# Kernel optimization log

Measured on AMD Instinct MI355X. Metric: run time of the kernel, lower is better.

Reference implementation:

```python
import jax, jax.numpy as jnp
import numpy as np

RADIUS = 5          # box-filter radius -> 11x11 kernel
TEMP = 0.5          # multinomial temperature
NSAMP = 5           # sampling_num
EPS = 1e-6
BN_EPS = 1e-5


def _conv(x, w, stride=1, padding=0, groups=1):
    return jax.lax.conv_general_dilated(
        x, w, window_strides=(stride, stride),
        padding=[(padding, padding), (padding, padding)],
        feature_group_count=groups,
        dimension_numbers=("NCHW", "OIHW", "NCHW"))


def custom_conv(x, w, key, stride=1, padding=0):
    """conv2d with cosine-activation regularization (bias=False path)."""
    B = x.shape[0]
    Cout = w.shape[0]
    # all-ones 'norm' conv on x*x
    x_norm = jnp.sqrt(_conv(x * x, jnp.ones_like(w), stride, padding))
    y = _conv(x, w, stride, padding)
    w_norm = jnp.sqrt(jnp.sum(w * w, axis=(1, 2, 3)))  # per-out-channel Frobenius norm
    cosine = y / (w_norm[None, :, None, None] + EPS) / (x_norm + EPS)
    # 11x11 depthwise box filter
    k = 2 * RADIUS + 1
    dw = jnp.ones((Cout, 1, k, k), x.dtype)
    cosine_mean = _conv(cosine, dw, 1, RADIUS, groups=Cout) / (k * k)
    H, W = cosine.shape[2], cosine.shape[3]
    # multinomial(NSAMP, exp(cosine/TEMP)) counts, no_grad in original
    logits = jax.lax.stop_gradient(cosine).reshape(B, Cout, H * W) / TEMP
    idx = jax.random.categorical(key, logits, axis=-1, shape=(NSAMP, B, Cout))
    bi = jnp.broadcast_to(jnp.arange(B)[None, :, None], (NSAMP, B, Cout))
    ci = jnp.broadcast_to(jnp.arange(Cout)[None, None, :], (NSAMP, B, Cout))
    mask = jnp.zeros((B, Cout, H * W), x.dtype).at[bi, ci, idx].add(1.0)
    cm = cosine_mean.reshape(B, Cout, H * W)
    act = ((mask * cm).sum(-1) / mask.sum(-1)).mean()
    return y, act


def batchnorm(x, g, b):
    # training-mode batch statistics (biased variance), like nn.BatchNorm2d
    m = x.mean(axis=(0, 2, 3), keepdims=True)
    v = x.var(axis=(0, 2, 3), keepdims=True)
    return (x - m) / jnp.sqrt(v + BN_EPS) * g[None, :, None, None] + b[None, :, None, None]


def setup_inputs() -> dict:
    key = jax.random.key(0)
    ks = jax.random.split(key, 10)
    x = jax.random.normal(ks[0], (16, 256, 56, 56), jnp.float32)
    w1 = jax.random.normal(ks[1], (64, 256, 1, 1), jnp.float32) * 0.05
    w2 = jax.random.normal(ks[2], (64, 64, 3, 3), jnp.float32) * 0.05
    w3 = jax.random.normal(ks[3], (256, 64, 1, 1), jnp.float32) * 0.05
    g1 = 1.0 + 0.05 * jax.random.normal(ks[4], (64,), jnp.float32)
    b1 = 0.05 * jax.random.normal(ks[5], (64,), jnp.float32)
    g2 = 1.0 + 0.05 * jax.random.normal(ks[6], (64,), jnp.float32)
    b2 = 0.05 * jax.random.normal(ks[7], (64,), jnp.float32)
    g3 = 1.0 + 0.05 * jax.random.normal(ks[8], (256,), jnp.float32)
    b3 = 0.05 * jax.random.normal(ks[9], (256,), jnp.float32)
    return {"x": x, "w1": w1, "w2": w2, "w3": w3,
            "g1": g1, "b1": b1, "g2": g2, "b2": b2, "g3": g3, "b3": b3}


def reference(x, w1, w2, w3, g1, b1, g2, b2, g3, b3):
    k0, k1, k2 = jax.random.split(jax.random.key(42), 3)
    acc = jnp.asarray(0.0, x.dtype)
    out, a = custom_conv(x, w1, k0)           # conv1x1
    acc = acc + a
    out = jax.nn.relu(batchnorm(out, g1, b1))
    out, a = custom_conv(out, w2, k1, padding=1)  # conv3x3, stride 1
    acc = acc + a
    out = jax.nn.relu(batchnorm(out, g2, b2))
    out, a = custom_conv(out, w3, k2)         # conv1x1 expand
    acc = acc + a
    out = batchnorm(out, g3, b3)
    out = jax.nn.relu(out + x)                # identity shortcut (downsample=None)
    return out, acc
```

## Files before the change

### kernel.cpp

```cpp
#include <hip/hip_runtime.h>
#include <stdint.h>
#include <math.h>

#define HW 3136
#define NPIX 50176

__device__ __forceinline__ int min_i(int a, int b) { return a < b ? a : b; }

typedef __attribute__((ext_vector_type(8))) short bf16x8;
typedef __attribute__((ext_vector_type(4))) float f32x4;
#define MFMA16(a, b, c) __builtin_amdgcn_mfma_f32_16x16x32_bf16(a, b, c, 0, 0, 0)

__device__ __forceinline__ unsigned short f2bf(float f) {
  unsigned u = __float_as_uint(f);
  u = (u + 0x7fffu + ((u >> 16) & 1u)) >> 16;
  return (unsigned short)u;
}
__device__ __forceinline__ unsigned pk2(float a, float b) {
  return (unsigned)f2bf(a) | ((unsigned)f2bf(b) << 16);
}
__device__ __forceinline__ float bf2f(unsigned short h) {
  return __uint_as_float(((unsigned)h) << 16);
}

#define ROTL32(v, r) __builtin_rotateleft32((uint32_t)(v), (r))

__host__ __device__ inline void threefry2x32(uint32_t k0, uint32_t k1,
                                             uint32_t x0, uint32_t x1,
                                             uint32_t& o0, uint32_t& o1) {
  uint32_t k2 = k0 ^ k1 ^ 0x1BD11BDAu;
  x0 += k0; x1 += k1;
  x0 += x1; x1 = ROTL32(x1, 13); x1 ^= x0;
  x0 += x1; x1 = ROTL32(x1, 15); x1 ^= x0;
  x0 += x1; x1 = ROTL32(x1, 26); x1 ^= x0;
  x0 += x1; x1 = ROTL32(x1, 6);  x1 ^= x0;
  x0 += k1; x1 += k2 + 1u;
  x0 += x1; x1 = ROTL32(x1, 17); x1 ^= x0;
  x0 += x1; x1 = ROTL32(x1, 29); x1 ^= x0;
  x0 += x1; x1 = ROTL32(x1, 16); x1 ^= x0;
  x0 += x1; x1 = ROTL32(x1, 24); x1 ^= x0;
  x0 += k2; x1 += k0 + 2u;
  x0 += x1; x1 = ROTL32(x1, 13); x1 ^= x0;
  x0 += x1; x1 = ROTL32(x1, 15); x1 ^= x0;
  x0 += x1; x1 = ROTL32(x1, 26); x1 ^= x0;
  x0 += x1; x1 = ROTL32(x1, 6);  x1 ^= x0;
  x0 += k0; x1 += k1 + 3u;
  x0 += x1; x1 = ROTL32(x1, 17); x1 ^= x0;
  x0 += x1; x1 = ROTL32(x1, 29); x1 ^= x0;
  x0 += x1; x1 = ROTL32(x1, 16); x1 ^= x0;
  x0 += x1; x1 = ROTL32(x1, 24); x1 ^= x0;
  x0 += k1; x1 += k2 + 4u;
  x0 += x1; x1 = ROTL32(x1, 13); x1 ^= x0;
  x0 += x1; x1 = ROTL32(x1, 15); x1 ^= x0;
  x0 += x1; x1 = ROTL32(x1, 26); x1 ^= x0;
  x0 += x1; x1 = ROTL32(x1, 6);  x1 ^= x0;
  x0 += k2; x1 += k0 + 5u;
  o0 = x0; o1 = x1;
}

#define TF5_R(r)                                            \
  _Pragma("unroll") for (int i = 0; i < 5; ++i) {           \
    x0[i] += x1[i]; x1[i] = ROTL32(x1[i], r) ^ x0[i];       \
  }
#define TF5_INJ(a, b)                                       \
  _Pragma("unroll") for (int i = 0; i < 5; ++i) {           \
    x0[i] += (a); x1[i] += (b);                             \
  }
__device__ __forceinline__ void threefry5(uint32_t k0, uint32_t k1,
    const uint32_t xa[5], const uint32_t xb[5], uint32_t oa[5], uint32_t ob[5]) {
  uint32_t k2 = k0 ^ k1 ^ 0x1BD11BDAu;
  uint32_t x0[5], x1[5];
  #pragma unroll
  for (int i = 0; i < 5; ++i) { x0[i] = xa[i] + k0; x1[i] = xb[i] + k1; }
  TF5_R(13) TF5_R(15) TF5_R(26) TF5_R(6)  TF5_INJ(k1, k2 + 1u)
  TF5_R(17) TF5_R(29) TF5_R(16) TF5_R(24) TF5_INJ(k2, k0 + 2u)
  TF5_R(13) TF5_R(15) TF5_R(26) TF5_R(6)  TF5_INJ(k0, k1 + 3u)
  TF5_R(17) TF5_R(29) TF5_R(16) TF5_R(24) TF5_INJ(k1, k2 + 4u)
  TF5_R(13) TF5_R(15) TF5_R(26) TF5_R(6)  TF5_INJ(k2, k0 + 5u)
  #pragma unroll
  for (int i = 0; i < 5; ++i) { oa[i] = x0[i]; ob[i] = x1[i]; }
}

#define NLN2F -0.6931471805599453f
#define NEG2LOG2E -2.8853900817779268f
__device__ __forceinline__ float exp_draw(uint32_t bits) {
  float u = __uint_as_float((bits >> 9) | 0x3f800000u) - 1.0f;
  u = fmaxf(u, 1.17549435e-38f);
  return NLN2F * __log2f(u);
}

template <int NT>
__device__ void sample5_body(const unsigned short* __restrict__ CS,
    float* __restrict__ acc, uint32_t key0, uint32_t key1, int BC, float scale,
    int u, unsigned* kmin, float* wsum) {
  const int v = u + (BC >> 1);
  const uint32_t sC = (uint32_t)BC * (uint32_t)HW;
  const uint32_t halfn = sC * 2u + (sC >> 1);
  const unsigned short* rowU = CS + (size_t)u * HW;
  const unsigned short* rowV = CS + (size_t)v * HW;
  const int tid = threadIdx.x;
  const int lane = tid & 63;

  if (tid < 10) { kmin[tid] = 0xFFFFFFFFu; wsum[tid] = 0.f; }

  unsigned bk[10];
  #pragma unroll
  for (int k = 0; k < 10; ++k) bk[k] = 0xFFFFFFFFu;

  const uint32_t baseU0 = (uint32_t)u * (uint32_t)HW;
  const uint32_t baseV0 = (uint32_t)v * (uint32_t)HW;
  for (int p = tid; p < HW; p += NT) {
    float wu = __builtin_amdgcn_exp2f(bf2f(rowU[p]) * NEG2LOG2E);
    float wv = __builtin_amdgcn_exp2f(bf2f(rowV[p]) * NEG2LOG2E);
    uint32_t eU = baseU0 + (uint32_t)p;
    uint32_t eV = baseV0 + (uint32_t)p;
    uint32_t xa[5] = {eU, eU + sC, eU + 2 * sC, eV, eV + sC};
    uint32_t xb[5] = {eU + halfn, eU + sC + halfn, eU + 2 * sC + halfn,
                      eV + halfn, eV + sC + halfn};
    uint32_t oa[5], ob[5];
    threefry5(key0, key1, xa, xb, oa, ob);
    uint32_t wds[10] = {oa[0], oa[1], oa[2], ob[3], ob[4],
                        oa[3], oa[4], ob[0], ob[1], ob[2]};
    #pragma unroll
    for (int k = 0; k < 10; ++k) {
      float s = exp_draw(wds[k]) * (k < 5 ? wu : wv);
      unsigned key = (__float_as_uint(s) & 0xFFFFF000u) | (unsigned)p;
      bk[k] = bk[k] < key ? bk[k] : key;
    }
  }

  __syncthreads();
  #pragma unroll
  for (int k = 0; k < 10; ++k) {
    unsigned kv = bk[k];
    #pragma unroll
    for (int o = 32; o; o >>= 1) {
      unsigned ov = __shfl_xor(kv, o);
      kv = kv < ov ? kv : ov;
    }
    if (lane == 0) atomicMin(&kmin[k], kv);
  }
  __syncthreads();

  for (int idx = tid; idx < 1210; idx += NT) {
    int win = idx / 121, j = idx - win * 121;
    int bidx = (int)(kmin[win] & 0xFFFu);
    int py = bidx / 56, px = bidx % 56;
    int yy = py + j / 11 - 5, xx = px + j % 11 - 5;
    if (yy >= 0 && yy < 56 && xx >= 0 && xx < 56) {
      const unsigned short* row = (win < 5) ? rowU : rowV;
      atomicAdd(&wsum[win], bf2f(row[yy * 56 + xx]));
    }
  }
  __syncthreads();
  if (tid == 0) {
    float t = 0.f;
    #pragma unroll
    for (int k = 0; k < 10; ++k) t += wsum[k];
    atomicAdd(acc, t * scale);
  }
}

template <int NT>
__global__ __launch_bounds__(NT) void sample5_k(const unsigned short* __restrict__ CS,
    float* __restrict__ acc, uint32_t key0, uint32_t key1, int BC, float scale) {
  __shared__ unsigned kmin[10];
  __shared__ float wsum[10];
  sample5_body<NT>(CS, acc, key0, key1, BC, scale, blockIdx.x, kmin, wsum);
}

__global__ void wprep_k(const float* __restrict__ w1, const float* __restrict__ w2,
                        const float* __restrict__ w3, float* __restrict__ invwn,
                        unsigned short* __restrict__ W1b, unsigned short* __restrict__ W2tb,
                        unsigned short* __restrict__ W3b) {
  int i = blockIdx.x * 256 + threadIdx.x;
  if (i < 16384) {
    W1b[i] = f2bf(w1[i]);
  } else if (i < 53248) {
    int o = i - 16384;
    int co = o / 576, r = o % 576, tap = r >> 6, ci = r & 63;
    W2tb[o] = f2bf(w2[co * 576 + ci * 9 + tap]);
  } else if (i < 69632) {
    int o = i - 53248;
    W3b[o] = f2bf(w3[o]);
  } else {
    int t = i - 69632;
    if (t < 64) {
      float s = 0.f;
      for (int k = 0; k < 256; k++) { float v = w1[t * 256 + k]; s = fmaf(v, v, s); }
      invwn[t] = 1.0f / (sqrtf(s) + 1e-6f);
    } else if (t < 128) {
      int c = t - 64; float s = 0.f;
      for (int k = 0; k < 576; k++) { float v = w2[c * 576 + k]; s = fmaf(v, v, s); }
      invwn[t] = 1.0f / (sqrtf(s) + 1e-6f);
    } else if (t < 384) {
      int c = t - 128; float s = 0.f;
      for (int k = 0; k < 64; k++) { float v = w3[c * 64 + k]; s = fmaf(v, v, s); }
      invwn[t] = 1.0f / (sqrtf(s) + 1e-6f);
    }
  }
}

__global__ __launch_bounds__(256) void bn_fin(const float* __restrict__ Sp,
    const float* __restrict__ Qp, const float* __restrict__ g,
    const float* __restrict__ b, float* __restrict__ sc, float* __restrict__ sh,
    int nblk) {
  const int c = blockIdx.x, tid = threadIdx.x;
  const float* rs = Sp + (size_t)c * nblk;
  const float* rq = Qp + (size_t)c * nblk;
  float s = 0.f, q = 0.f;
  for (int i = tid; i < nblk; i += 256) { s += rs[i]; q += rq[i]; }
  #pragma unroll
  for (int o = 32; o; o >>= 1) { s += __shfl_xor(s, o); q += __shfl_xor(q, o); }
  __shared__ float S[4], Q[4];
  int lane = tid & 63, wave = tid >> 6;
  if (lane == 0) { S[wave] = s; Q[wave] = q; }
  __syncthreads();
  if (tid == 0) {
    float st = S[0] + S[1] + S[2] + S[3];
    float qt = Q[0] + Q[1] + Q[2] + Q[3];
    float mean = st * (1.0f / (float)NPIX);
    float var = qt * (1.0f / (float)NPIX) - mean * mean;
    float sv = g[c] / sqrtf(var + 1e-5f);
    sc[c] = sv; sh[c] = b[c] - mean * sv;
  }
}

__global__ __launch_bounds__(256) void conv1_mfma(
    const float* __restrict__ X, const unsigned short* __restrict__ Wb,
    const float* __restrict__ invwn, unsigned short* __restrict__ Y1,
    unsigned short* __restrict__ CS, float* __restrict__ Sp, float* __restrict__ Qp) {
#define ST1 264
#define NB1 784
  __shared__ __align__(16) unsigned short bq[64 * ST1];
  __shared__ float sqp[4][64];
  __shared__ float ixn[64];
  const int p0 = blockIdx.x * 64, b = blockIdx.y;
  const int bid = b * 49 + blockIdx.x;
  const int tid = threadIdx.x;
  const int lane = tid & 63, wave = tid >> 6;
  const int m = lane & 15, quad = lane >> 4;
  const int co0 = wave * 16;
  const float* Xb = X + (size_t)b * 256 * HW + p0;

  bf16x8 afr[8];
  const unsigned short* wrow = Wb + (co0 + m) * 256 + quad * 8;
  #pragma unroll
  for (int k = 0; k < 8; ++k) afr[k] = *(const bf16x8*)(wrow + k * 32);

  {
    const int px = tid & 63, rg = tid >> 6;
    float sq = 0.f;
    #pragma unroll
    for (int it = 0; it < 16; ++it) {
      int ci = rg * 64 + it * 4;
      float v0 = Xb[(size_t)(ci + 0) * HW + px];
      float v1 = Xb[(size_t)(ci + 1) * HW + px];
      float v2 = Xb[(size_t)(ci + 2) * HW + px];
      float v3 = Xb[(size_t)(ci + 3) * HW + px];
      sq += v0 * v0 + v1 * v1 + v2 * v2 + v3 * v3;
      *(uint2*)&bq[px * ST1 + ci] = make_uint2(pk2(v0, v1), pk2(v2, v3));
    }
    sqp[rg][px] = sq;
  }
  __syncthreads();
  if (tid < 64)
    ixn[tid] = 1.0f / (sqrtf(sqp[0][tid] + sqp[1][tid] + sqp[2][tid] + sqp[3][tid]) + 1e-6f);
  __syncthreads();

  f32x4 acc[4];
  #pragma unroll
  for (int nt = 0; nt < 4; ++nt) acc[nt] = (f32x4)0.f;
  #pragma unroll
  for (int nt = 0; nt < 4; ++nt) {
    const unsigned short* brow = &bq[(nt * 16 + m) * ST1 + quad * 8];
    #pragma unroll
    for (int k = 0; k < 8; ++k) {
      bf16x8 bfrag = *(const bf16x8*)(brow + k * 32);
      acc[nt] = MFMA16(afr[k], bfrag, acc[nt]);
    }
  }

  float s[4] = {0, 0, 0, 0}, q[4] = {0, 0, 0, 0};
  #pragma unroll
  for (int nt = 0; nt < 4; ++nt) {
    int px = nt * 16 + m;
    size_t bp = (size_t)b * HW + p0 + px;
    float ix = ixn[px];
    *(uint2*)&Y1[bp * 64 + co0 + quad * 4] =
        make_uint2(pk2(acc[nt][0], acc[nt][1]), pk2(acc[nt][2], acc[nt][3]));
    #pragma unroll
    for (int r = 0; r < 4; ++r) {
      int co = co0 + quad * 4 + r;
      float v = acc[nt][r];
      CS[((size_t)b * 64 + co) * HW + p0 + px] = f2bf(v * invwn[co] * ix);
      s[r] += v; q[r] = fmaf(v, v, q[r]);
    }
  }
  #pragma unroll
  for (int r = 0; r < 4; ++r) {
    float ss = s[r], qq = q[r];
    #pragma unroll
    for (int o = 8; o; o >>= 1) { ss += __shfl_xor(ss, o); qq += __shfl_xor(qq, o); }
    if (m == 0) {
      int co = co0 + quad * 4 + r;
      Sp[(size_t)co * NB1 + bid] = ss; Qp[(size_t)co * NB1 + bid] = qq;
    }
  }
#undef NB1
#undef ST1
}

__global__ __launch_bounds__(256) void chansum_px(const unsigned short* __restrict__ Y1,
    const float* __restrict__ sc, const float* __restrict__ sh,
    float* __restrict__ part) {
  int g = blockIdx.x * 256 + threadIdx.x;
  const unsigned short* row = Y1 + (size_t)g * 64;
  float s = 0.f;
  #pragma unroll
  for (int j = 0; j < 8; ++j) {
    uint4 d = *(const uint4*)(row + j * 8);
    unsigned dd[4] = {d.x, d.y, d.z, d.w};
    #pragma unroll
    for (int e = 0; e < 4; ++e) {
      int c = j * 8 + e * 2;
      float v0 = fmaxf(0.f, fmaf(bf2f((unsigned short)(dd[e] & 0xffff)), sc[c], sh[c]));
      float v1 = fmaxf(0.f, fmaf(bf2f((unsigned short)(dd[e] >> 16)), sc[c + 1], sh[c + 1]));
      s = fmaf(v0, v0, s); s = fmaf(v1, v1, s);
    }
  }
  part[g] = s;
}

__global__ __launch_bounds__(256) void box3inv(const float* __restrict__ part,
                                               float* __restrict__ out) {
  int g = blockIdx.x * 256 + threadIdx.x;
  int b = g / HW, p = g - b * HW;
  int y = p / 56, x = p % 56;
  float tot = 0.f;
  for (int dy = -1; dy <= 1; dy++) {
    int yy = y + dy; if (yy < 0 || yy >= 56) continue;
    for (int dx = -1; dx <= 1; dx++) {
      int xx = x + dx; if (xx < 0 || xx >= 56) continue;
      tot += part[b * HW + yy * 56 + xx];
    }
  }
  out[g] = 1.0f / (sqrtf(tot) + 1e-6f);
}

__global__ __launch_bounds__(256) void conv2_mfma(
    const unsigned short* __restrict__ Y1, const unsigned short* __restrict__ W2tb,
    const float* __restrict__ invwn, const float* __restrict__ ixn2,
    const float* __restrict__ sc1, const float* __restrict__ sh1,
    unsigned short* __restrict__ Y2, unsigned short* __restrict__ CS,
    float* __restrict__ Sp, float* __restrict__ Qp) {
#define STW 72
#define NB2 896
  __shared__ __align__(16) unsigned short ts[3 * 66 * STW];
  __shared__ float scl[64], shl[64];
  const int h = blockIdx.x, b = blockIdx.y;
  const int bid = b * 56 + h;
  const int tid = threadIdx.x;
  const int lane = tid & 63, wave = tid >> 6;
  const int m = lane & 15, quad = lane >> 4;
  const int co0 = wave * 16;
  if (tid < 64) { scl[tid] = sc1[tid]; shl[tid] = sh1[tid]; }

  bf16x8 afr[18];
  #pragma unroll
  for (int ks = 0; ks < 18; ++ks)
    afr[ks] = *(const bf16x8*)(W2tb + (co0 + m) * 576 + ks * 32 + quad * 8);
  __syncthreads();

  for (int l = tid; l < 6336; l += 256) {
    int cp = l & 31, cc = (l >> 5) % 66, dy = l / 2112;
    int yy = h - 1 + dy, xx = cc - 1;
    unsigned pkv = 0u;
    if (yy >= 0 && yy < 56 && xx >= 0 && xx < 56) {
      unsigned d = *(const unsigned*)&Y1[((size_t)b * HW + yy * 56 + xx) * 64 + cp * 2];
      float v0 = bf2f((unsigned short)(d & 0xffff));
      float v1 = bf2f((unsigned short)(d >> 16));
      v0 = fmaxf(0.f, fmaf(v0, scl[cp * 2], shl[cp * 2]));
      v1 = fmaxf(0.f, fmaf(v1, scl[cp * 2 + 1], shl[cp * 2 + 1]));
      pkv = pk2(v0, v1);
    }
    *(unsigned*)&ts[(dy * 66 + cc) * STW + cp * 2] = pkv;
  }
  __syncthreads();

  f32x4 acc[4];
  #pragma unroll
  for (int nt = 0; nt < 4; ++nt) acc[nt] = (f32x4)0.f;
  #pragma unroll
  for (int nt = 0; nt < 4; ++nt) {
    #pragma unroll
    for (int ks = 0; ks < 18; ++ks) {
      int tap = ks >> 1, half = ks & 1;
      int dy = tap / 3, dx = tap % 3;
      bf16x8 bfrag = *(const bf16x8*)&ts[(dy * 66 + nt * 16 + m + dx) * STW + half * 32 + quad * 8];
      acc[nt] = MFMA16(afr[ks], bfrag, acc[nt]);
    }
  }

  float s[4] = {0, 0, 0, 0}, q[4] = {0, 0, 0, 0};
  #pragma unroll
  for (int nt = 0; nt < 4; ++nt) {
    int px = nt * 16 + m;
    bool valid = px < 56;
    int pix = h * 56 + px;
    if (valid) {
      float ix = ixn2[b * HW + pix];
      size_t bp = (size_t)b * HW + pix;
      *(uint2*)&Y2[bp * 64 + co0 + quad * 4] =
          make_uint2(pk2(acc[nt][0], acc[nt][1]), pk2(acc[nt][2], acc[nt][3]));
      #pragma unroll
      for (int r = 0; r < 4; ++r) {
        int co = co0 + quad * 4 + r;
        CS[((size_t)b * 64 + co) * HW + pix] = f2bf(acc[nt][r] * invwn[co] * ix);
      }
    }
    #pragma unroll
    for (int r = 0; r < 4; ++r) {
      float v = valid ? acc[nt][r] : 0.f;
      s[r] += v; q[r] = fmaf(v, v, q[r]);
    }
  }
  #pragma unroll
  for (int r = 0; r < 4; ++r) {
    float ss = s[r], qq = q[r];
    #pragma unroll
    for (int o = 8; o; o >>= 1) { ss += __shfl_xor(ss, o); qq += __shfl_xor(qq, o); }
    if (m == 0) {
      int co = co0 + quad * 4 + r;
      Sp[(size_t)co * NB2 + bid] = ss; Qp[(size_t)co * NB2 + bid] = qq;
    }
  }
#undef NB2
#undef STW
}

__global__ __launch_bounds__(256) void conv3_mfma(
    const unsigned short* __restrict__ Y2, const unsigned short* __restrict__ W3b,
    const float* __restrict__ invwn,
    const float* __restrict__ sc2, const float* __restrict__ sh2,
    unsigned short* __restrict__ Y3, unsigned short* __restrict__ CS,
    float* __restrict__ Sp, float* __restrict__ Qp) {
#define ST3 72
#define NB3 784
  __shared__ __align__(16) unsigned short bq[64 * ST3];
  __shared__ float scl[64], shl[64], sqp[4][64], ixn[64];
  const int p0 = blockIdx.x * 64, b = blockIdx.y;
  const int bid = b * 49 + blockIdx.x;
  const int tid = threadIdx.x;
  const int lane = tid & 63, wave = tid >> 6;
  const int m = lane & 15, quad = lane >> 4;
  const int co0 = wave * 64;
  if (tid < 64) { scl[tid] = sc2[tid]; shl[tid] = sh2[tid]; }

  bf16x8 afr[4][2];
  #pragma unroll
  for (int mt = 0; mt < 4; ++mt)
    #pragma unroll
    for (int k = 0; k < 2; ++k)
      afr[mt][k] = *(const bf16x8*)(W3b + (co0 + mt * 16 + m) * 64 + k * 32 + quad * 8);
  __syncthreads();

  {
    const int cp = tid & 31, pxg = tid >> 5;
    #pragma unroll
    for (int it = 0; it < 8; ++it) {
      int px = pxg * 8 + it;
      unsigned d = *(const unsigned*)&Y2[((size_t)b * HW + p0 + px) * 64 + cp * 2];
      float v0 = bf2f((unsigned short)(d & 0xffff));
      float v1 = bf2f((unsigned short)(d >> 16));
      v0 = fmaxf(0.f, fmaf(v0, scl[cp * 2], shl[cp * 2]));
      v1 = fmaxf(0.f, fmaf(v1, scl[cp * 2 + 1], shl[cp * 2 + 1]));
      *(unsigned*)&bq[px * ST3 + cp * 2] = pk2(v0, v1);
    }
  }
  __syncthreads();
  {
    const int px = tid & 63, hh = tid >> 6;
    const unsigned short* row = &bq[px * ST3 + hh * 16];
    float sq = 0.f;
    #pragma unroll
    for (int e = 0; e < 16; ++e) { float v = bf2f(row[e]); sq = fmaf(v, v, sq); }
    sqp[hh][px] = sq;
  }
  __syncthreads();
  if (tid < 64)
    ixn[tid] = 1.0f / (sqrtf(sqp[0][tid] + sqp[1][tid] + sqp[2][tid] + sqp[3][tid]) + 1e-6f);
  __syncthreads();

  f32x4 acc[4][4];
  #pragma unroll
  for (int mt = 0; mt < 4; ++mt)
    #pragma unroll
    for (int nt = 0; nt < 4; ++nt) acc[mt][nt] = (f32x4)0.f;
  #pragma unroll
  for (int nt = 0; nt < 4; ++nt) {
    const unsigned short* brow = &bq[(nt * 16 + m) * ST3 + quad * 8];
    bf16x8 b0 = *(const bf16x8*)(brow);
    bf16x8 b1 = *(const bf16x8*)(brow + 32);
    #pragma unroll
    for (int mt = 0; mt < 4; ++mt) {
      acc[mt][nt] = MFMA16(afr[mt][0], b0, acc[mt][nt]);
      acc[mt][nt] = MFMA16(afr[mt][1], b1, acc[mt][nt]);
    }
  }

  #pragma unroll
  for (int mt = 0; mt < 4; ++mt) {
    float s[4] = {0, 0, 0, 0}, q[4] = {0, 0, 0, 0};
    #pragma unroll
    for (int nt = 0; nt < 4; ++nt) {
      int px = nt * 16 + m;
      float ix = ixn[px];
      #pragma unroll
      for (int r = 0; r < 4; ++r) {
        int co = co0 + mt * 16 + quad * 4 + r;
        float v = acc[mt][nt][r];
        size_t off = ((size_t)b * 256 + co) * HW + p0 + px;
        Y3[off] = f2bf(v);
        CS[off] = f2bf(v * invwn[co] * ix);
        s[r] += v; q[r] = fmaf(v, v, q[r]);
      }
    }
    #pragma unroll
    for (int r = 0; r < 4; ++r) {
      float ss = s[r], qq = q[r];
      #pragma unroll
      for (int o = 8; o; o >>= 1) { ss += __shfl_xor(ss, o); qq += __shfl_xor(qq, o); }
      if (m == 0) {
        int co = co0 + mt * 16 + quad * 4 + r;
        Sp[(size_t)co * NB3 + bid] = ss; Qp[(size_t)co * NB3 + bid] = qq;
      }
    }
  }
#undef NB3
#undef ST3
}

__global__ __launch_bounds__(256, 8) void final_samp_fused(
    const unsigned short* __restrict__ Y3, const float* __restrict__ X,
    const float* __restrict__ sc, const float* __restrict__ sh,
    float* __restrict__ out, const unsigned short* __restrict__ CS3,
    float* __restrict__ accp, uint32_t key0, uint32_t key1, float scale,
    int NS, int R) {
  __shared__ unsigned kmin[10];
  __shared__ float wsum[10];
  const int g = blockIdx.x;
  if ((g % R) == 0 && (g / R) < NS) {
    sample5_body<256>(CS3, accp, key0, key1, 4096, scale, g / R, kmin, wsum);
    return;
  }
  const int fb = g - min_i((g + R - 1) / R, NS);
  size_t i4 = (size_t)fb * 256 + threadIdx.x;
  size_t i = i4 * 4;
  int c = (int)((i / HW) % 256);
  float a = sc[c], d = sh[c];
  uint2 yd = *(const uint2*)&Y3[i];
  float4 xv = *(const float4*)&X[i];
  float4 r;
  r.x = fmaxf(0.f, fmaf(bf2f((unsigned short)(yd.x & 0xffff)), a, d) + xv.x);
  r.y = fmaxf(0.f, fmaf(bf2f((unsigned short)(yd.x >> 16)),    a, d) + xv.y);
  r.z = fmaxf(0.f, fmaf(bf2f((unsigned short)(yd.y & 0xffff)), a, d) + xv.z);
  r.w = fmaxf(0.f, fmaf(bf2f((unsigned short)(yd.y >> 16)),    a, d) + xv.w);
  *(float4*)&out[i] = r;
}

__global__ void acc_write_k(const float* __restrict__ accp, float* __restrict__ out) {
  out[12845056] = accp[0];
}

extern "C" void kernel_launch(void* const* d_in, const int* in_sizes, int n_in,
                              void* d_out, int out_size, void* d_ws, size_t ws_size,
                              hipStream_t stream) {
  (void)in_sizes; (void)n_in; (void)out_size; (void)ws_size;
  const float* x  = (const float*)d_in[0];
  const float* w1 = (const float*)d_in[1];
  const float* w2 = (const float*)d_in[2];
  const float* w3 = (const float*)d_in[3];
  const float* g1 = (const float*)d_in[4];
  const float* b1 = (const float*)d_in[5];
  const float* g2 = (const float*)d_in[6];
  const float* b2 = (const float*)d_in[7];
  const float* g3 = (const float*)d_in[8];
  const float* b3 = (const float*)d_in[9];
  float* out = (float*)d_out;
  float* ws = (float*)d_ws;

  size_t o = 0;
  unsigned short* y3b  = (unsigned short*)(ws + o); o += 6422528;
  unsigned short* cos3 = (unsigned short*)(ws + o); o += 6422528;
  unsigned short* CSb  = (unsigned short*)(ws + o); o += 1605632;
  unsigned short* y1b  = (unsigned short*)(ws + o); o += 1605632;
  unsigned short* y2b  = (unsigned short*)(ws + o); o += 1605632;
  unsigned short* W1b  = (unsigned short*)(ws + o); o += 8192;
  unsigned short* W2tb = (unsigned short*)(ws + o); o += 18432;
  unsigned short* W3b  = (unsigned short*)(ws + o); o += 8192;
  float* part = ws + o; o += NPIX;
  float* ixn2 = ws + o; o += NPIX;
  float* invwn = ws + o; o += 384;
  float* Sp1 = ws + o; o += 64 * 784;   float* Qp1 = ws + o; o += 64 * 784;
  float* Sp2 = ws + o; o += 64 * 896;   float* Qp2 = ws + o; o += 64 * 896;
  float* Sp3 = ws + o; o += 256 * 784;  float* Qp3 = ws + o; o += 256 * 784;
  float* acc = ws + o; o += 1;
  float* sc1 = ws + o; o += 64;  float* sh1 = ws + o; o += 64;
  float* sc2 = ws + o; o += 64;  float* sh2 = ws + o; o += 64;
  float* sc3 = ws + o; o += 256; float* sh3 = ws + o; o += 256;

  hipMemsetAsync(acc, 0, sizeof(float), stream);

  uint32_t A0, B0, A1, B1, A2, B2;
  threefry2x32(0u, 42u, 0u, 3u, A0, B0);
  threefry2x32(0u, 42u, 1u, 4u, A1, B1);
  threefry2x32(0u, 42u, 2u, 5u, A2, B2);

  const float scale64  = 1.0f / (121.0f * 5.0f * 1024.0f);
  const float scale256 = 1.0f / (121.0f * 5.0f * 4096.0f);

  wprep_k<<<274, 256, 0, stream>>>(w1, w2, w3, invwn, W1b, W2tb, W3b);

  conv1_mfma<<<dim3(49, 16), 256, 0, stream>>>(x, W1b, invwn, y1b, CSb, Sp1, Qp1);
  bn_fin<<<64, 256, 0, stream>>>(Sp1, Qp1, g1, b1, sc1, sh1, 784);
  sample5_k<512><<<512, 512, 0, stream>>>(CSb, acc, A0, A1, 1024, scale64);

  chansum_px<<<196, 256, 0, stream>>>(y1b, sc1, sh1, part);
  box3inv<<<196, 256, 0, stream>>>(part, ixn2);
  conv2_mfma<<<dim3(56, 16), 256, 0, stream>>>(
      y1b, W2tb, invwn + 64, ixn2, sc1, sh1, y2b, CSb, Sp2, Qp2);
  bn_fin<<<64, 256, 0, stream>>>(Sp2, Qp2, g2, b2, sc2, sh2, 896);
  sample5_k<512><<<512, 512, 0, stream>>>(CSb, acc, A2, B0, 1024, scale64);

  conv3_mfma<<<dim3(49, 16), 256, 0, stream>>>(
      y2b, W3b, invwn + 128, sc2, sh2, y3b, cos3, Sp3, Qp3);
  bn_fin<<<256, 256, 0, stream>>>(Sp3, Qp3, g3, b3, sc3, sh3, 784);

  final_samp_fused<<<14592, 256, 0, stream>>>(
      y3b, x, sc3, sh3, out, cos3, acc, B1, B2, scale256, 2048, 2);
  acc_write_k<<<1, 1, 0, stream>>>(acc, out);
}
```

Before: 451.6 us.

## Defer all three sampling passes into one fused final kernel

When the workspace is large enough, the conv2 cosine map goes to a separate buffer, so the two stage-1/2 sampling launches can be deferred. All three multinomial sampling passes then run in one final kernel alongside the BN+residual+ReLU elementwise work. This removes two serialized launches and lets sampling overlap the bandwidth-bound epilogue. In exchange it uses more workspace, and each sampling block loops over two (batch, channel) pairs with 256 threads instead of 512.

Result: faster. 402.4 us (-10.9%).

```diff
diff --git a/kernel.cpp b/kernel.cpp
--- a/kernel.cpp
+++ b/kernel.cpp
@@ -4,8 +4,6 @@
 
 #define HW 3136
 #define NPIX 50176
-
-__device__ __forceinline__ int min_i(int a, int b) { return a < b ? a : b; }
 
 typedef __attribute__((ext_vector_type(8))) short bf16x8;
 typedef __attribute__((ext_vector_type(4))) float f32x4;
@@ -169,6 +167,47 @@
   sample5_body<NT>(CS, acc, key0, key1, BC, scale, blockIdx.x, kmin, wsum);
 }
 
+__global__ __launch_bounds__(256, 8) void mega_k(
+    const unsigned short* __restrict__ CS1, const unsigned short* __restrict__ CS2,
+    const unsigned short* __restrict__ CS3,
+    const unsigned short* __restrict__ Y3, const float* __restrict__ X,
+    const float* __restrict__ sc, const float* __restrict__ sh,
+    float* __restrict__ out, float* __restrict__ accp,
+    uint32_t A0, uint32_t A1, uint32_t A2, uint32_t B0, uint32_t B1, uint32_t B2,
+    float s64, float s256, int pairStart, int pairEnd, int nSampBlk, int NF) {
+  __shared__ unsigned kmin[10];
+  __shared__ float wsum[10];
+  const int g = blockIdx.x;
+  if (g < nSampBlk) {
+    for (int pi = pairStart + g; pi < pairEnd; pi += nSampBlk) {
+      if (pi < 512)
+        sample5_body<256>(CS1, accp, A0, A1, 1024, s64, pi, kmin, wsum);
+      else if (pi < 1024)
+        sample5_body<256>(CS2, accp, A2, B0, 1024, s64, pi - 512, kmin, wsum);
+      else
+        sample5_body<256>(CS3, accp, B1, B2, 4096, s256, pi - 1024, kmin, wsum);
+    }
+    return;
+  }
+  const int fb = g - nSampBlk;
+  if (fb >= NF) return;
+  size_t i = ((size_t)fb * 256 + threadIdx.x) * 4;
+  int c = (int)((i / HW) % 256);
+  float a = sc[c], d = sh[c];
+  uint2 yd = *(const uint2*)&Y3[i];
+  float4 xv = *(const float4*)&X[i];
+  float4 r;
+  r.x = fmaxf(0.f, fmaf(bf2f((unsigned short)(yd.x & 0xffff)), a, d) + xv.x);
+  r.y = fmaxf(0.f, fmaf(bf2f((unsigned short)(yd.x >> 16)),    a, d) + xv.y);
+  r.z = fmaxf(0.f, fmaf(bf2f((unsigned short)(yd.y & 0xffff)), a, d) + xv.z);
+  r.w = fmaxf(0.f, fmaf(bf2f((unsigned short)(yd.y >> 16)),    a, d) + xv.w);
+  *(float4*)&out[i] = r;
+}
+
+__global__ void acc_write_k(const float* __restrict__ accp, float* __restrict__ out) {
+  out[12845056] = accp[0];
+}
+
 __global__ void wprep_k(const float* __restrict__ w1, const float* __restrict__ w2,
                         const float* __restrict__ w3, float* __restrict__ invwn,
                         unsigned short* __restrict__ W1b, unsigned short* __restrict__ W2tb,
@@ -541,42 +580,10 @@
 #undef ST3
 }
 
-__global__ __launch_bounds__(256, 8) void final_samp_fused(
-    const unsigned short* __restrict__ Y3, const float* __restrict__ X,
-    const float* __restrict__ sc, const float* __restrict__ sh,
-    float* __restrict__ out, const unsigned short* __restrict__ CS3,
-    float* __restrict__ accp, uint32_t key0, uint32_t key1, float scale,
-    int NS, int R) {
-  __shared__ unsigned kmin[10];
-  __shared__ float wsum[10];
-  const int g = blockIdx.x;
-  if ((g % R) == 0 && (g / R) < NS) {
-    sample5_body<256>(CS3, accp, key0, key1, 4096, scale, g / R, kmin, wsum);
-    return;
-  }
-  const int fb = g - min_i((g + R - 1) / R, NS);
-  size_t i4 = (size_t)fb * 256 + threadIdx.x;
-  size_t i = i4 * 4;
-  int c = (int)((i / HW) % 256);
-  float a = sc[c], d = sh[c];
-  uint2 yd = *(const uint2*)&Y3[i];
-  float4 xv = *(const float4*)&X[i];
-  float4 r;
-  r.x = fmaxf(0.f, fmaf(bf2f((unsigned short)(yd.x & 0xffff)), a, d) + xv.x);
-  r.y = fmaxf(0.f, fmaf(bf2f((unsigned short)(yd.x >> 16)),    a, d) + xv.y);
-  r.z = fmaxf(0.f, fmaf(bf2f((unsigned short)(yd.y & 0xffff)), a, d) + xv.z);
-  r.w = fmaxf(0.f, fmaf(bf2f((unsigned short)(yd.y >> 16)),    a, d) + xv.w);
-  *(float4*)&out[i] = r;
-}
-
-__global__ void acc_write_k(const float* __restrict__ accp, float* __restrict__ out) {
-  out[12845056] = accp[0];
-}
-
 extern "C" void kernel_launch(void* const* d_in, const int* in_sizes, int n_in,
                               void* d_out, int out_size, void* d_ws, size_t ws_size,
                               hipStream_t stream) {
-  (void)in_sizes; (void)n_in; (void)out_size; (void)ws_size;
+  (void)in_sizes; (void)n_in; (void)out_size;
   const float* x  = (const float*)d_in[0];
   const float* w1 = (const float*)d_in[1];
   const float* w2 = (const float*)d_in[2];
@@ -610,6 +617,9 @@
   float* sc2 = ws + o; o += 64;  float* sh2 = ws + o; o += 64;
   float* sc3 = ws + o; o += 256; float* sh3 = ws + o; o += 256;
 
+  const bool big = ws_size >= (o + 1605632) * sizeof(float);
+  unsigned short* CS2b = big ? (unsigned short*)(ws + o) : CSb;
+
   hipMemsetAsync(acc, 0, sizeof(float), stream);
 
   uint32_t A0, B0, A1, B1, A2, B2;
@@ -624,20 +634,27 @@
 
   conv1_mfma<<<dim3(49, 16), 256, 0, stream>>>(x, W1b, invwn, y1b, CSb, Sp1, Qp1);
   bn_fin<<<64, 256, 0, stream>>>(Sp1, Qp1, g1, b1, sc1, sh1, 784);
-  sample5_k<512><<<512, 512, 0, stream>>>(CSb, acc, A0, A1, 1024, scale64);
-
+  if (!big)
+    sample5_k<512><<<512, 512, 0, stream>>>(CSb, acc, A0, A1, 1024, scale64);
   chansum_px<<<196, 256, 0, stream>>>(y1b, sc1, sh1, part);
   box3inv<<<196, 256, 0, stream>>>(part, ixn2);
   conv2_mfma<<<dim3(56, 16), 256, 0, stream>>>(
-      y1b, W2tb, invwn + 64, ixn2, sc1, sh1, y2b, CSb, Sp2, Qp2);
+      y1b, W2tb, invwn + 64, ixn2, sc1, sh1, y2b, CS2b, Sp2, Qp2);
   bn_fin<<<64, 256, 0, stream>>>(Sp2, Qp2, g2, b2, sc2, sh2, 896);
-  sample5_k<512><<<512, 512, 0, stream>>>(CSb, acc, A2, B0, 1024, scale64);
-
+  if (!big)
+    sample5_k<512><<<512, 512, 0, stream>>>(CS2b, acc, A2, B0, 1024, scale64);
   conv3_mfma<<<dim3(49, 16), 256, 0, stream>>>(
       y2b, W3b, invwn + 128, sc2, sh2, y3b, cos3, Sp3, Qp3);
   bn_fin<<<256, 256, 0, stream>>>(Sp3, Qp3, g3, b3, sc3, sh3, 784);
 
-  final_samp_fused<<<14592, 256, 0, stream>>>(
-      y3b, x, sc3, sh3, out, cos3, acc, B1, B2, scale256, 2048, 2);
+  if (big) {
+    mega_k<<<1536 + 12544, 256, 0, stream>>>(
+        CSb, CS2b, cos3, y3b, x, sc3, sh3, out, acc,
+        A0, A1, A2, B0, B1, B2, scale64, scale256, 0, 3072, 1536, 12544);
+  } else {
+    mega_k<<<1024 + 12544, 256, 0, stream>>>(
+        CSb, CS2b, cos3, y3b, x, sc3, sh3, out, acc,
+        A0, A1, A2, B0, B1, B2, scale64, scale256, 1024, 3072, 1024, 12544);
+  }
   acc_write_k<<<1, 1, 0, stream>>>(acc, out);
 }
```
